# Optimization experiments

Hardware: AMD Instinct MI355X
Metric: run time of the kernel (lower is better)

Reference implementation:

```python
import jax, jax.numpy as jnp
import numpy as np

VAR = (0.1, 0.2)        # SSD encoding variances
THRESH = 0.5            # overlap_thresh
NEGPOS = 3              # neg:pos ratio


def _point_form(p):
    # (cx,cy,w,h) -> (x1,y1,x2,y2)
    return jnp.concatenate([p[:, :2] - p[:, 2:] / 2, p[:, :2] + p[:, 2:] / 2], axis=1)


def _jaccard(a, b):
    # a: [O,4], b: [P,4], corner form -> IoU [O,P]
    lt = jnp.maximum(a[:, None, :2], b[None, :, :2])
    rb = jnp.minimum(a[:, None, 2:], b[None, :, 2:])
    wh = jnp.maximum(rb - lt, 0.0)
    inter = wh[..., 0] * wh[..., 1]
    area_a = ((a[:, 2] - a[:, 0]) * (a[:, 3] - a[:, 1]))[:, None]
    area_b = ((b[:, 2] - b[:, 0]) * (b[:, 3] - b[:, 1]))[None, :]
    return inter / (area_a + area_b - inter)


def _encode(matched, priors):
    # matched: [P,4] corner form, priors: [P,4] center form
    g_cxcy = ((matched[:, :2] + matched[:, 2:]) / 2 - priors[:, :2]) / (VAR[0] * priors[:, 2:])
    g_wh = jnp.log((matched[:, 2:] - matched[:, :2]) / priors[:, 2:]) / VAR[1]
    return jnp.concatenate([g_cxcy, g_wh], axis=1)


def _match(truths, labels, priors):
    # truths: [O,4], labels: [O], priors: [P,4] -> loc_t [P,4], conf_t [P], obj_t [P]
    O = truths.shape[0]
    over = _jaccard(truths, _point_form(priors))          # [O,P]
    best_prior_idx = jnp.argmax(over, axis=1)             # [O] best prior per truth
    best_truth_overlap = over.max(axis=0)                 # [P]
    best_truth_idx = jnp.argmax(over, axis=0)             # [P]
    best_truth_overlap = best_truth_overlap.at[best_prior_idx].set(2.0)
    best_truth_idx = best_truth_idx.at[best_prior_idx].set(jnp.arange(O))
    matched = truths[best_truth_idx]                      # [P,4]
    conf = labels[best_truth_idx].astype(jnp.int32) + 1   # background = 0
    conf = jnp.where(best_truth_overlap < THRESH, 0, conf)
    return _encode(matched, priors), conf, conf > 0


def _ce(logits, tgt):
    # per-element cross entropy, logits [...,C], tgt [...] int
    return jax.nn.logsumexp(logits, axis=-1) - jnp.take_along_axis(logits, tgt[..., None], axis=-1)[..., 0]


def _mine_neg(loss, pos, P):
    # hard negative mining via double argsort (rank of each elem in descending loss order)
    loss = jnp.where(pos, 0.0, loss)
    loss_idx = jnp.argsort(-loss, axis=1)
    idx_rank = jnp.argsort(loss_idx, axis=1)
    num_neg = jnp.minimum(NEGPOS * pos.sum(axis=1, keepdims=True), P - 1)
    return idx_rank < num_neg


def setup_inputs() -> dict:
    key = jax.random.key(0)
    ks = jax.random.split(key, 8)
    B, P, C, O = 64, 16320, 81, 50
    loc_data = jax.random.normal(ks[0], (B, P, 4), jnp.float32)
    conf_data = jax.random.normal(ks[1], (B, P, C), jnp.float32)
    obj_data = jax.random.normal(ks[2], (B, P, 2), jnp.float32)
    # priors: center form, positive w/h
    cxcy = jax.random.uniform(ks[3], (P, 2), minval=0.05, maxval=0.95)
    wh = jax.random.uniform(ks[4], (P, 2), minval=0.02, maxval=0.3)
    priors = jnp.concatenate([cxcy, wh], axis=1).astype(jnp.float32)
    # targets: valid corner-form boxes + float label in last column
    tc = jax.random.uniform(ks[5], (B, O, 2), minval=0.1, maxval=0.9)
    twh = jax.random.uniform(ks[6], (B, O, 2), minval=0.05, maxval=0.3)
    boxes = jnp.concatenate([jnp.clip(tc - twh / 2, 0.0, 1.0), jnp.clip(tc + twh / 2, 0.0, 1.0)], axis=-1)
    labels = jax.random.randint(ks[7], (B, O), 0, C).astype(jnp.float32)
    targets = jnp.concatenate([boxes, labels[..., None]], axis=-1).astype(jnp.float32)
    return {"loc_data": loc_data, "conf_data": conf_data, "obj_data": obj_data,
            "priors": priors, "targets": targets}


def reference(loc_data, conf_data, obj_data, priors, targets):
    B, P, C = conf_data.shape
    loc_t, conf_t, pos = jax.vmap(lambda t: _match(t[:, :4], t[:, 4], priors))(targets)
    loc_t = jax.lax.stop_gradient(loc_t)  # torch builds targets detached

    # localization: smooth L1 over positives, sum reduction
    d = loc_data - loc_t
    sl1 = jnp.where(jnp.abs(d) < 1.0, 0.5 * d * d, jnp.abs(d) - 0.5)
    loss_l = jnp.sum(sl1 * pos[..., None].astype(sl1.dtype))

    # combined (C+1)-way logit: col0 = obj_bg + log(sum(exp(conf))), cols 1..C = obj_fg + conf
    lse_conf = jax.nn.logsumexp(conf_data, axis=-1)                        # [B,P]
    logit = jnp.concatenate([(obj_data[..., 0] + lse_conf)[..., None],
                             obj_data[..., 1:2] + conf_data], axis=-1)     # [B,P,C+1]

    ce_c = _ce(logit, conf_t)                       # [B,P]
    neg_c = _mine_neg(ce_c, pos, P)
    loss_c = jnp.sum(jnp.where(pos | neg_c, ce_c, 0.0))

    ce_o = _ce(obj_data, pos.astype(jnp.int32))     # [B,P]
    neg_o = _mine_neg(ce_o, pos, P)
    loss_obj = jnp.sum(jnp.where(pos | neg_o, ce_o, 0.0))

    N = pos.sum().astype(jnp.float32)
    return loss_l / N, loss_c / N, loss_obj / N
```

## Files before the change

kernel.cpp:

```cpp
#include <hip/hip_runtime.h>
#include <cstdint>
#include <cstddef>

#define THRESH   0.5f
#define NEGPOS   3
#define VAR0     0.1f
#define VAR1     0.2f
#define MAXO     64
#define NPRI     8
#define A1_T     256
#define MINE_T   1024
#define MINE_W   (MINE_T / 64)
#define HCOPIES  8

__global__ __launch_bounds__(A1_T)
void match_kernel(const float* __restrict__ priors,
                  const float* __restrict__ targets,
                  unsigned char* __restrict__ code,
                  unsigned long long* __restrict__ g_bp,
                  int B, int P, int O, int chunks) {
    __shared__ float tx1[MAXO], ty1[MAXO], tx2[MAXO], ty2[MAXO], tarea[MAXO];
    const int b   = blockIdx.x / chunks;
    const int ch  = blockIdx.x % chunks;
    const int tid = threadIdx.x;

    if (tid < O) {
        const float* tr = targets + (size_t)(b * O + tid) * 5;
        float x1 = tr[0], y1 = tr[1], x2 = tr[2], y2 = tr[3];
        tx1[tid] = x1; ty1[tid] = y1; tx2[tid] = x2; ty2[tid] = y2;
        tarea[tid] = (x2 - x1) * (y2 - y1);
    }
    __syncthreads();

    float px1[NPRI], py1[NPRI], px2[NPRI], py2[NPRI], pa[NPRI], pov[NPRI];
    int   pidx[NPRI];
    const int p0 = ch * (A1_T * NPRI) + tid;
#pragma unroll
    for (int i = 0; i < NPRI; ++i) {
        int p = p0 + i * A1_T;
        pov[i] = -1.0f; pidx[i] = 0;
        px1[i] = 0.f; py1[i] = 0.f; px2[i] = 0.f; py2[i] = 0.f; pa[i] = 1.0f;
        if (p < P) {
            float4 pr = *(const float4*)(priors + (size_t)p * 4);
            px1[i] = pr.x - pr.z * 0.5f; py1[i] = pr.y - pr.w * 0.5f;
            px2[i] = pr.x + pr.z * 0.5f; py2[i] = pr.y + pr.w * 0.5f;
            pa[i]  = pr.z * pr.w;
        }
    }

    const int lane = tid & 63;
    for (int o = 0; o < O; ++o) {
        float ax1 = tx1[o], ay1 = ty1[o], ax2 = tx2[o], ay2 = ty2[o], aa = tarea[o];
        float bo = -1.0f; unsigned bp = 0u;
#pragma unroll
        for (int i = 0; i < NPRI; ++i) {
            float lx = fmaxf(ax1, px1[i]), ly = fmaxf(ay1, py1[i]);
            float rx = fminf(ax2, px2[i]), ry = fminf(ay2, py2[i]);
            float w = fmaxf(rx - lx, 0.0f), h = fmaxf(ry - ly, 0.0f);
            float inter = w * h;
            float iou = __fdividef(inter, aa + pa[i] - inter);
            if (iou > pov[i]) { pov[i] = iou; pidx[i] = o; }
            if (iou > bo)     { bo = iou; bp = (unsigned)(p0 + i * A1_T); }
        }
        unsigned long long key =
            ((unsigned long long)__float_as_uint(bo) << 32) |
            (unsigned long long)(0xFFFFFFFFu - bp);
#pragma unroll
        for (int d = 1; d < 64; d <<= 1) {
            unsigned long long other = __shfl_xor(key, d, 64);
            if (other > key) key = other;
        }
        if (lane == 0)
            atomicMax(&g_bp[(size_t)b * O + o], key);
    }

#pragma unroll
    for (int i = 0; i < NPRI; ++i) {
        int p = p0 + i * A1_T;
        if (p < P)
            code[(size_t)b * P + p] =
                (pov[i] >= THRESH) ? (unsigned char)(pidx[i] + 1) : (unsigned char)0;
    }
}

__global__ void force_kernel(const unsigned long long* __restrict__ g_bp,
                             unsigned char* __restrict__ code,
                             int B, int P, int O) {
    int b = blockIdx.x * blockDim.x + threadIdx.x;
    if (b >= B) return;
    for (int o = 0; o < O; ++o) {
        unsigned long long key = g_bp[(size_t)b * O + o];
        unsigned p = 0xFFFFFFFFu - (unsigned)(key & 0xFFFFFFFFull);
        code[(size_t)b * P + p] = (unsigned char)(o + 1);
    }
}

__global__ __launch_bounds__(256)
void ce_pos_kernel(const float* __restrict__ loc, const float* __restrict__ conf,
                   const float* __restrict__ obj, const float* __restrict__ priors,
                   const float* __restrict__ targets,
                   const unsigned char* __restrict__ code,
                   float* __restrict__ mce, float* __restrict__ rowacc,
                   int B, int P, int C, int O) {
    const int b = blockIdx.y;
    const int p = blockIdx.x * 256 + threadIdx.x;
    const int tid = threadIdx.x, wv = tid >> 6, lane = tid & 63;

    bool pos = false;
    unsigned cc = 0;
    const unsigned t = (unsigned)(b * P + p);
    float obx = 0.f, oby = 0.f, lse2 = 0.f;
    if (p < P) {
        cc = code[t];
        float2 ob = *(const float2*)(obj + (size_t)t * 2);
        obx = ob.x; oby = ob.y;
        float m = fmaxf(obx, oby);
        lse2 = m + __logf(__expf(obx - m) + __expf(oby - m));
        if (cc == 0) {
            mce[t] = lse2 - obx;
        } else {
            mce[t] = 0.0f;
            pos = true;
        }
    }

    const unsigned long long msk = __ballot(pos);
    float myS = 0.f;
    unsigned long long rem = msk;
    while (rem) {
        const int src = __ffsll(rem) - 1;
        rem &= rem - 1;
        const unsigned t_s = (unsigned)__shfl((int)t, src, 64);
        const float* cr = conf + (size_t)t_s * C;
        float s = 0.f;
        for (int j = lane; j < C; j += 64) s += __expf(cr[j]);
#pragma unroll
        for (int d = 1; d < 64; d <<= 1) s += __shfl_xor(s, d, 64);
        if (lane == src) myS = s;
    }

    float sl = 0.f, cec = 0.f, ceo = 0.f;
    if (pos) {
        const float* cr = conf + (size_t)t * C;
        const float* tr = targets + (size_t)((unsigned)(b * O) + cc - 1u) * 5;
        float4 pr = *(const float4*)(priors + (size_t)p * 4);
        float4 ld = *(const float4*)(loc + (size_t)t * 4);
        float mx1 = tr[0], my1 = tr[1], mx2 = tr[2], my2 = tr[3];
        int   lbl = (int)tr[4];

        float lsec = __logf(myS);
        cec = lsec + lse2 - oby - cr[lbl];
        ceo = lse2 - oby;

        float gx  = ((mx1 + mx2) * 0.5f - pr.x) / (VAR0 * pr.z);
        float gy  = ((my1 + my2) * 0.5f - pr.y) / (VAR0 * pr.w);
        float gw2 = __logf((mx2 - mx1) / pr.z) / VAR1;
        float gh  = __logf((my2 - my1) / pr.w) / VAR1;
        float d0 = ld.x - gx,  a0 = fabsf(d0); sl += (a0 < 1.f) ? 0.5f * d0 * d0 : a0 - 0.5f;
        float d1 = ld.y - gy,  a1 = fabsf(d1); sl += (a1 < 1.f) ? 0.5f * d1 * d1 : a1 - 0.5f;
        float d2 = ld.z - gw2, a2 = fabsf(d2); sl += (a2 < 1.f) ? 0.5f * d2 * d2 : a2 - 0.5f;
        float d3 = ld.w - gh,  a3 = fabsf(d3); sl += (a3 < 1.f) ? 0.5f * d3 * d3 : a3 - 0.5f;
    }

    float cntp = (float)__popcll(msk);
    __shared__ float red[4][4];
#pragma unroll
    for (int d = 32; d > 0; d >>= 1) {
        sl  += __shfl_down(sl,  d, 64);
        cec += __shfl_down(cec, d, 64);
        ceo += __shfl_down(ceo, d, 64);
    }
    if (lane == 0) {
        red[wv][0] = cntp; red[wv][1] = sl; red[wv][2] = cec; red[wv][3] = ceo;
    }
    __syncthreads();
    if (tid < 4) {
        float v = red[0][tid] + red[1][tid] + red[2][tid] + red[3][tid];
        if (v != 0.0f)
            atomicAdd(rowacc + (size_t)b * 16 + tid, v);
    }
}

__global__ __launch_bounds__(MINE_T)
void mine_kernel(const float* __restrict__ mce, const float* __restrict__ rowacc,
                 float* __restrict__ g_neg, int P) {
    const int b = blockIdx.x;
    const float* row = mce + (size_t)b * P;
    int npos = (int)rowacc[(size_t)b * 16];
    int k = NEGPOS * npos;
    if (k > P - 1) k = P - 1;
    if (k <= 0) return;

    __shared__ unsigned hist[HCOPIES][257];
    __shared__ unsigned s_prefix;
    __shared__ int      s_rem;
    __shared__ float    s_ws[MINE_W];
    __shared__ int      s_wc[MINE_W];

    const int tid  = threadIdx.x;
    const int wv   = tid >> 6;
    const int hc   = wv & (HCOPIES - 1);
    const int lane = tid & 63;

    unsigned prefix = 0u;
    int rem = k;
    for (int shift = 24; shift >= 0; shift -= 8) {
        for (int i = tid; i < HCOPIES * 257; i += MINE_T) (&hist[0][0])[i] = 0u;
        __syncthreads();
        unsigned himask = (shift == 24) ? 0u : (0xFFFFFFFFu << (shift + 8));
        for (int i = tid; i < P; i += MINE_T) {
            unsigned bits = __float_as_uint(row[i]);
            if ((bits & himask) == prefix)
                atomicAdd(&hist[hc][(bits >> shift) & 0xFFu], 1u);
        }
        __syncthreads();
        if (tid == 0) {
            int cum = 0; unsigned bin = 0;
            for (int bb = 255; bb >= 0; --bb) {
                int cnt = 0;
#pragma unroll
                for (int h = 0; h < HCOPIES; ++h) cnt += (int)hist[h][bb];
                if (cum + cnt >= rem) { bin = (unsigned)bb; rem -= cum; break; }
                cum += cnt;
            }
            s_prefix = prefix | (bin << shift);
            s_rem = rem;
        }
        __syncthreads();
        prefix = s_prefix;
        rem    = s_rem;
    }

    float vk = __uint_as_float(prefix);
    float s = 0.f; int cnt = 0;
    for (int i = tid; i < P; i += MINE_T) {
        float v = row[i];
        if (__float_as_uint(v) > prefix) { s += v; ++cnt; }
    }
#pragma unroll
    for (int d = 32; d > 0; d >>= 1) {
        s   += __shfl_down(s, d, 64);
        cnt += __shfl_down(cnt, d, 64);
    }
    if (lane == 0) { s_ws[wv] = s; s_wc[wv] = cnt; }
    __syncthreads();
    if (tid == 0) {
        float st = 0.f; int ct = 0;
        for (int w = 0; w < MINE_W; ++w) { st += s_ws[w]; ct += s_wc[w]; }
        atomicAdd(g_neg, st + (float)(k - ct) * vk);
    }
}

__global__ void finish_kernel(const float* __restrict__ rowacc,
                              const float* __restrict__ g_neg,
                              float* __restrict__ out, int B) {
    const int lane = threadIdx.x;
    float npos = 0.f, sl = 0.f, cec = 0.f, ceo = 0.f;
    for (int b = lane; b < B; b += 64) {
        float4 v = *(const float4*)(rowacc + (size_t)b * 16);
        npos += v.x; sl += v.y; cec += v.z; ceo += v.w;
    }
#pragma unroll
    for (int d = 32; d > 0; d >>= 1) {
        npos += __shfl_down(npos, d, 64);
        sl   += __shfl_down(sl,   d, 64);
        cec  += __shfl_down(cec,  d, 64);
        ceo  += __shfl_down(ceo,  d, 64);
    }
    if (lane == 0) {
        float neg = *g_neg;
        out[0] = sl / npos;
        out[1] = (cec + neg) / npos;
        out[2] = (ceo + neg) / npos;
    }
}

extern "C" void kernel_launch(void* const* d_in, const int* in_sizes, int n_in,
                              void* d_out, int out_size, void* d_ws, size_t ws_size,
                              hipStream_t stream) {
    const float* loc     = (const float*)d_in[0];
    const float* conf    = (const float*)d_in[1];
    const float* obj     = (const float*)d_in[2];
    const float* priors  = (const float*)d_in[3];
    const float* targets = (const float*)d_in[4];

    const int P = in_sizes[3] / 4;
    const int B = in_sizes[0] / (4 * P);
    const int C = in_sizes[1] / (B * P);
    const int O = in_sizes[4] / (5 * B);

    char* ws = (char*)d_ws;
    size_t off = 0;
    float* g_neg = (float*)(ws + off);             off += 64;
    float* rowacc = (float*)(ws + off);            off += (size_t)B * 16 * sizeof(float);
    unsigned long long* g_bp = (unsigned long long*)(ws + off);
    off += (size_t)B * O * sizeof(unsigned long long);
    const size_t zero_bytes = off;
    off = (off + 127) & ~(size_t)127;
    unsigned char* code = (unsigned char*)(ws + off); off += (size_t)B * P;
    off = (off + 127) & ~(size_t)127;
    float* mce = (float*)(ws + off);               off += (size_t)B * P * sizeof(float);

    hipMemsetAsync(d_ws, 0, zero_bytes, stream);

    const int chunks = (P + A1_T * NPRI - 1) / (A1_T * NPRI);
    match_kernel<<<B * chunks, A1_T, 0, stream>>>(priors, targets, code, g_bp,
                                                  B, P, O, chunks);
    force_kernel<<<(B + 63) / 64, 64, 0, stream>>>(g_bp, code, B, P, O);
    dim3 ce_grid((P + 255) / 256, B);
    ce_pos_kernel<<<ce_grid, 256, 0, stream>>>(loc, conf, obj, priors, targets,
                                               code, mce, rowacc, B, P, C, O);
    mine_kernel<<<B, MINE_T, 0, stream>>>(mce, rowacc, g_neg, P);
    finish_kernel<<<1, 64, 0, stream>>>(rowacc, g_neg, (float*)d_out, B);
}
```

Measured before the change: 585.6 us.

## Fuse CE and hard-negative mining into one per-row kernel with value histogram

```diff
diff --git a/kernel.cpp b/kernel.cpp
--- a/kernel.cpp
+++ b/kernel.cpp
@@ -9,20 +9,22 @@
 #define MAXO     64
 #define NPRI     8
 #define A1_T     256
-#define MINE_T   1024
-#define MINE_W   (MINE_T / 64)
-#define HCOPIES  8
+#define ROW_T    1024
+#define NBIN     4096
+#define CAP      4096
 
 __global__ __launch_bounds__(A1_T)
 void match_kernel(const float* __restrict__ priors,
                   const float* __restrict__ targets,
                   unsigned char* __restrict__ code,
-                  unsigned long long* __restrict__ g_bp,
+                  unsigned long long* __restrict__ g_bp2,
                   int B, int P, int O, int chunks) {
     __shared__ float tx1[MAXO], ty1[MAXO], tx2[MAXO], ty2[MAXO], tarea[MAXO];
+    __shared__ unsigned long long wkeys[(A1_T / 64) * MAXO];
     const int b   = blockIdx.x / chunks;
     const int ch  = blockIdx.x % chunks;
     const int tid = threadIdx.x;
+    const int lane = tid & 63, wv = tid >> 6;
 
     if (tid < O) {
         const float* tr = targets + (size_t)(b * O + tid) * 5;
@@ -48,7 +50,6 @@
         }
     }
 
-    const int lane = tid & 63;
     for (int o = 0; o < O; ++o) {
         float ax1 = tx1[o], ay1 = ty1[o], ax2 = tx2[o], ay2 = ty2[o], aa = tarea[o];
         float bo = -1.0f; unsigned bp = 0u;
@@ -70,8 +71,17 @@
             unsigned long long other = __shfl_xor(key, d, 64);
             if (other > key) key = other;
         }
-        if (lane == 0)
-            atomicMax(&g_bp[(size_t)b * O + o], key);
+        if (lane == 0) wkeys[wv * MAXO + o] = key;
+    }
+    __syncthreads();
+    if (tid < O) {
+        unsigned long long k = wkeys[tid];
+#pragma unroll
+        for (int w = 1; w < A1_T / 64; ++w) {
+            unsigned long long o2 = wkeys[w * MAXO + tid];
+            if (o2 > k) k = o2;
+        }
+        g_bp2[(size_t)(b * chunks + ch) * MAXO + tid] = k;
     }
 
 #pragma unroll
@@ -83,182 +93,211 @@
     }
 }
 
-__global__ void force_kernel(const unsigned long long* __restrict__ g_bp,
-                             unsigned char* __restrict__ code,
-                             int B, int P, int O) {
-    int b = blockIdx.x * blockDim.x + threadIdx.x;
-    if (b >= B) return;
-    for (int o = 0; o < O; ++o) {
-        unsigned long long key = g_bp[(size_t)b * O + o];
-        unsigned p = 0xFFFFFFFFu - (unsigned)(key & 0xFFFFFFFFull);
-        code[(size_t)b * P + p] = (unsigned char)(o + 1);
-    }
-}
-
-__global__ __launch_bounds__(256)
-void ce_pos_kernel(const float* __restrict__ loc, const float* __restrict__ conf,
-                   const float* __restrict__ obj, const float* __restrict__ priors,
-                   const float* __restrict__ targets,
-                   const unsigned char* __restrict__ code,
-                   float* __restrict__ mce, float* __restrict__ rowacc,
-                   int B, int P, int C, int O) {
-    const int b = blockIdx.y;
-    const int p = blockIdx.x * 256 + threadIdx.x;
-    const int tid = threadIdx.x, wv = tid >> 6, lane = tid & 63;
-
-    bool pos = false;
-    unsigned cc = 0;
-    const unsigned t = (unsigned)(b * P + p);
-    float obx = 0.f, oby = 0.f, lse2 = 0.f;
-    if (p < P) {
-        cc = code[t];
-        float2 ob = *(const float2*)(obj + (size_t)t * 2);
-        obx = ob.x; oby = ob.y;
-        float m = fmaxf(obx, oby);
-        lse2 = m + __logf(__expf(obx - m) + __expf(oby - m));
+__global__ __launch_bounds__(64)
+void force_kernel(const unsigned long long* __restrict__ g_bp2,
+                  unsigned char* __restrict__ code,
+                  int P, int O, int chunks) {
+    const int b = blockIdx.x, o = threadIdx.x;
+    __shared__ unsigned s_p[MAXO];
+    unsigned p = 0xFFFFFFFFu;
+    if (o < O) {
+        unsigned long long k = 0ull;
+        for (int ch = 0; ch < chunks; ++ch) {
+            unsigned long long v = g_bp2[(size_t)(b * chunks + ch) * MAXO + o];
+            if (v > k) k = v;
+        }
+        p = 0xFFFFFFFFu - (unsigned)(k & 0xFFFFFFFFull);
+        s_p[o] = p;
+    }
+    __syncthreads();
+    if (o < O) {
+        bool last = true;
+        for (int o2 = o + 1; o2 < O; ++o2)
+            if (s_p[o2] == p) { last = false; break; }
+        if (last) code[(size_t)b * P + p] = (unsigned char)(o + 1);
+    }
+}
+
+__global__ __launch_bounds__(ROW_T)
+void row_kernel(const float* __restrict__ loc, const float* __restrict__ conf,
+                const float* __restrict__ obj, const float* __restrict__ priors,
+                const float* __restrict__ targets,
+                const unsigned char* __restrict__ code,
+                float* __restrict__ rowout, int P, int C, int O) {
+    const int b = blockIdx.x;
+    const int tid = threadIdx.x;
+    const int lane = tid & 63, wv = tid >> 6;
+
+    __shared__ unsigned hist[NBIN];
+    __shared__ int s_idx[CAP];
+    __shared__ int s_np, s_nc, s_bound, s_rem;
+    __shared__ int wavetot[ROW_T / 64], wexc[ROW_T / 64];
+    __shared__ float red[ROW_T / 64][4];
+
+    for (int i = tid; i < NBIN; i += ROW_T) hist[i] = 0u;
+    if (tid == 0) { s_np = 0; s_nc = 0; s_bound = NBIN; s_rem = 0; }
+    __syncthreads();
+
+    const size_t rowbase = (size_t)b * P;
+
+    for (int i = tid; i < P; i += ROW_T) {
+        unsigned cc = code[rowbase + i];
+        float2 ob = *(const float2*)(obj + (rowbase + i) * 2);
+        float m = fmaxf(ob.x, ob.y);
+        float lse2 = m + __logf(__expf(ob.x - m) + __expf(ob.y - m));
+        float v = 0.0f;
         if (cc == 0) {
-            mce[t] = lse2 - obx;
+            v = lse2 - ob.x;
         } else {
-            mce[t] = 0.0f;
-            pos = true;
-        }
-    }
-
-    const unsigned long long msk = __ballot(pos);
-    float myS = 0.f;
-    unsigned long long rem = msk;
-    while (rem) {
-        const int src = __ffsll(rem) - 1;
-        rem &= rem - 1;
-        const unsigned t_s = (unsigned)__shfl((int)t, src, 64);
-        const float* cr = conf + (size_t)t_s * C;
-        float s = 0.f;
-        for (int j = lane; j < C; j += 64) s += __expf(cr[j]);
-#pragma unroll
-        for (int d = 1; d < 64; d <<= 1) s += __shfl_xor(s, d, 64);
-        if (lane == src) myS = s;
-    }
-
-    float sl = 0.f, cec = 0.f, ceo = 0.f;
-    if (pos) {
-        const float* cr = conf + (size_t)t * C;
-        const float* tr = targets + (size_t)((unsigned)(b * O) + cc - 1u) * 5;
-        float4 pr = *(const float4*)(priors + (size_t)p * 4);
-        float4 ld = *(const float4*)(loc + (size_t)t * 4);
-        float mx1 = tr[0], my1 = tr[1], mx2 = tr[2], my2 = tr[3];
-        int   lbl = (int)tr[4];
-
-        float lsec = __logf(myS);
-        cec = lsec + lse2 - oby - cr[lbl];
-        ceo = lse2 - oby;
-
-        float gx  = ((mx1 + mx2) * 0.5f - pr.x) / (VAR0 * pr.z);
-        float gy  = ((my1 + my2) * 0.5f - pr.y) / (VAR0 * pr.w);
-        float gw2 = __logf((mx2 - mx1) / pr.z) / VAR1;
-        float gh  = __logf((my2 - my1) / pr.w) / VAR1;
-        float d0 = ld.x - gx,  a0 = fabsf(d0); sl += (a0 < 1.f) ? 0.5f * d0 * d0 : a0 - 0.5f;
-        float d1 = ld.y - gy,  a1 = fabsf(d1); sl += (a1 < 1.f) ? 0.5f * d1 * d1 : a1 - 0.5f;
-        float d2 = ld.z - gw2, a2 = fabsf(d2); sl += (a2 < 1.f) ? 0.5f * d2 * d2 : a2 - 0.5f;
-        float d3 = ld.w - gh,  a3 = fabsf(d3); sl += (a3 < 1.f) ? 0.5f * d3 * d3 : a3 - 0.5f;
-    }
-
-    float cntp = (float)__popcll(msk);
-    __shared__ float red[4][4];
+            int s = atomicAdd(&s_np, 1);
+            if (s < CAP) s_idx[s] = (i << 8) | (int)cc;
+        }
+        int bin = (int)(v * 512.0f);
+        bin = min(bin, NBIN - 1);
+        atomicAdd(&hist[bin], 1u);
+    }
+    __syncthreads();
+    const int np = s_np;
+
+    float sl = 0.f, cec = 0.f, ceo = 0.f, neg = 0.f;
+
+    {
+        const int unit = tid >> 4, lq = tid & 15;
+        for (int j = unit; j < np; j += ROW_T / 16) {
+            int pk = s_idx[j];
+            int p  = pk >> 8, cc = pk & 0xFF;
+            size_t t = rowbase + (size_t)p;
+            const float* cr = conf + t * C;
+            float s = 0.f;
+            for (int c = lq; c < C; c += 16) s += __expf(cr[c]);
+#pragma unroll
+            for (int d = 1; d < 16; d <<= 1) s += __shfl_xor(s, d, 16);
+            if (lq == 0) {
+                const float* tr = targets + (size_t)(b * O + cc - 1) * 5;
+                float2 ob = *(const float2*)(obj + t * 2);
+                float m = fmaxf(ob.x, ob.y);
+                float lse2 = m + __logf(__expf(ob.x - m) + __expf(ob.y - m));
+                int lbl = (int)tr[4];
+                cec += __logf(s) + lse2 - ob.y - cr[lbl];
+                ceo += lse2 - ob.y;
+                float4 pr = *(const float4*)(priors + (size_t)p * 4);
+                float4 ld = *(const float4*)(loc + t * 4);
+                float mx1 = tr[0], my1 = tr[1], mx2 = tr[2], my2 = tr[3];
+                float gx  = ((mx1 + mx2) * 0.5f - pr.x) / (VAR0 * pr.z);
+                float gy  = ((my1 + my2) * 0.5f - pr.y) / (VAR0 * pr.w);
+                float gw2 = __logf((mx2 - mx1) / pr.z) / VAR1;
+                float gh  = __logf((my2 - my1) / pr.w) / VAR1;
+                float d0 = ld.x - gx,  a0 = fabsf(d0); sl += (a0 < 1.f) ? 0.5f*d0*d0 : a0 - 0.5f;
+                float d1 = ld.y - gy,  a1 = fabsf(d1); sl += (a1 < 1.f) ? 0.5f*d1*d1 : a1 - 0.5f;
+                float d2 = ld.z - gw2, a2 = fabsf(d2); sl += (a2 < 1.f) ? 0.5f*d2*d2 : a2 - 0.5f;
+                float d3 = ld.w - gh,  a3 = fabsf(d3); sl += (a3 < 1.f) ? 0.5f*d3*d3 : a3 - 0.5f;
+            }
+        }
+    }
+    __syncthreads();
+
+    int k = NEGPOS * np;
+    if (k > P - 1) k = P - 1;
+    if (k > 0) {
+        const int base = NBIN - 1 - 4 * tid;
+        const int c0 = (int)hist[base],     c1 = (int)hist[base - 1];
+        const int c2 = (int)hist[base - 2], c3 = (int)hist[base - 3];
+        const int T = c0 + c1 + c2 + c3;
+        int incl = T;
+#pragma unroll
+        for (int d = 1; d < 64; d <<= 1) {
+            int vv = __shfl_up(incl, d, 64);
+            if (lane >= d) incl += vv;
+        }
+        if (lane == 63) wavetot[wv] = incl;
+        __syncthreads();
+        if (wv == 0 && lane < ROW_T / 64) {
+            int t2 = wavetot[lane], inc2 = t2;
+#pragma unroll
+            for (int d = 1; d < 16; d <<= 1) {
+                int vv = __shfl_up(inc2, d, 16);
+                if ((lane & 15) >= d) inc2 += vv;
+            }
+            wexc[lane] = inc2 - t2;
+        }
+        __syncthreads();
+        const int E = wexc[wv] + incl - T;
+        if (E < k && E + T >= k) {
+            int bound, rem;
+            if      (E + c0 >= k)           { bound = base;     rem = k - E; }
+            else if (E + c0 + c1 >= k)      { bound = base - 1; rem = k - E - c0; }
+            else if (E + c0 + c1 + c2 >= k) { bound = base - 2; rem = k - E - c0 - c1; }
+            else                            { bound = base - 3; rem = k - E - c0 - c1 - c2; }
+            s_bound = bound; s_rem = rem;
+        }
+    }
+    __syncthreads();
+    const int bound = s_bound, rem = s_rem;
+
+    if (k > 0) {
+        for (int i = tid; i < P; i += ROW_T) {
+            unsigned cc = code[rowbase + i];
+            if (cc) continue;
+            float2 ob = *(const float2*)(obj + (rowbase + i) * 2);
+            float m = fmaxf(ob.x, ob.y);
+            float v = m + __logf(__expf(ob.x - m) + __expf(ob.y - m)) - ob.x;
+            int bin = (int)(v * 512.0f);
+            bin = min(bin, NBIN - 1);
+            if (bin > bound) {
+                neg += v;
+            } else if (bin == bound) {
+                int c = atomicAdd(&s_nc, 1);
+                if (c < CAP) s_idx[c] = __float_as_int(v);
+            }
+        }
+    }
+    __syncthreads();
+
+    if (k > 0) {
+        int n = s_nc; if (n > CAP) n = CAP;
+        if (n <= rem) {
+            for (int i = tid; i < n; i += ROW_T) neg += __int_as_float(s_idx[i]);
+        } else {
+            for (int i = tid; i < n; i += ROW_T) {
+                unsigned bi = (unsigned)s_idx[i];
+                int g = 0, e = 0;
+                for (int j = 0; j < n; ++j) {
+                    unsigned bj = (unsigned)s_idx[j];
+                    g += (bj > bi);
+                    e += (j < i && bj == bi);
+                }
+                if (g + e < rem) neg += __int_as_float((int)bi);
+            }
+        }
+    }
+
 #pragma unroll
     for (int d = 32; d > 0; d >>= 1) {
         sl  += __shfl_down(sl,  d, 64);
         cec += __shfl_down(cec, d, 64);
         ceo += __shfl_down(ceo, d, 64);
-    }
-    if (lane == 0) {
-        red[wv][0] = cntp; red[wv][1] = sl; red[wv][2] = cec; red[wv][3] = ceo;
-    }
-    __syncthreads();
-    if (tid < 4) {
-        float v = red[0][tid] + red[1][tid] + red[2][tid] + red[3][tid];
-        if (v != 0.0f)
-            atomicAdd(rowacc + (size_t)b * 16 + tid, v);
-    }
-}
-
-__global__ __launch_bounds__(MINE_T)
-void mine_kernel(const float* __restrict__ mce, const float* __restrict__ rowacc,
-                 float* __restrict__ g_neg, int P) {
-    const int b = blockIdx.x;
-    const float* row = mce + (size_t)b * P;
-    int npos = (int)rowacc[(size_t)b * 16];
-    int k = NEGPOS * npos;
-    if (k > P - 1) k = P - 1;
-    if (k <= 0) return;
-
-    __shared__ unsigned hist[HCOPIES][257];
-    __shared__ unsigned s_prefix;
-    __shared__ int      s_rem;
-    __shared__ float    s_ws[MINE_W];
-    __shared__ int      s_wc[MINE_W];
-
-    const int tid  = threadIdx.x;
-    const int wv   = tid >> 6;
-    const int hc   = wv & (HCOPIES - 1);
-    const int lane = tid & 63;
-
-    unsigned prefix = 0u;
-    int rem = k;
-    for (int shift = 24; shift >= 0; shift -= 8) {
-        for (int i = tid; i < HCOPIES * 257; i += MINE_T) (&hist[0][0])[i] = 0u;
-        __syncthreads();
-        unsigned himask = (shift == 24) ? 0u : (0xFFFFFFFFu << (shift + 8));
-        for (int i = tid; i < P; i += MINE_T) {
-            unsigned bits = __float_as_uint(row[i]);
-            if ((bits & himask) == prefix)
-                atomicAdd(&hist[hc][(bits >> shift) & 0xFFu], 1u);
-        }
-        __syncthreads();
-        if (tid == 0) {
-            int cum = 0; unsigned bin = 0;
-            for (int bb = 255; bb >= 0; --bb) {
-                int cnt = 0;
-#pragma unroll
-                for (int h = 0; h < HCOPIES; ++h) cnt += (int)hist[h][bb];
-                if (cum + cnt >= rem) { bin = (unsigned)bb; rem -= cum; break; }
-                cum += cnt;
-            }
-            s_prefix = prefix | (bin << shift);
-            s_rem = rem;
-        }
-        __syncthreads();
-        prefix = s_prefix;
-        rem    = s_rem;
-    }
-
-    float vk = __uint_as_float(prefix);
-    float s = 0.f; int cnt = 0;
-    for (int i = tid; i < P; i += MINE_T) {
-        float v = row[i];
-        if (__float_as_uint(v) > prefix) { s += v; ++cnt; }
-    }
-#pragma unroll
-    for (int d = 32; d > 0; d >>= 1) {
-        s   += __shfl_down(s, d, 64);
-        cnt += __shfl_down(cnt, d, 64);
-    }
-    if (lane == 0) { s_ws[wv] = s; s_wc[wv] = cnt; }
+        neg += __shfl_down(neg, d, 64);
+    }
+    if (lane == 0) { red[wv][0] = sl; red[wv][1] = cec; red[wv][2] = ceo; red[wv][3] = neg; }
     __syncthreads();
     if (tid == 0) {
-        float st = 0.f; int ct = 0;
-        for (int w = 0; w < MINE_W; ++w) { st += s_ws[w]; ct += s_wc[w]; }
-        atomicAdd(g_neg, st + (float)(k - ct) * vk);
-    }
-}
-
-__global__ void finish_kernel(const float* __restrict__ rowacc,
-                              const float* __restrict__ g_neg,
-                              float* __restrict__ out, int B) {
+        float a0 = 0.f, a1 = 0.f, a2 = 0.f, a3 = 0.f;
+        for (int w = 0; w < ROW_T / 64; ++w) {
+            a0 += red[w][0]; a1 += red[w][1]; a2 += red[w][2]; a3 += red[w][3];
+        }
+        float* ro = rowout + (size_t)b * 8;
+        ro[0] = (float)np; ro[1] = a0; ro[2] = a1; ro[3] = a2; ro[4] = a3;
+    }
+}
+
+__global__ __launch_bounds__(64)
+void finish_kernel(const float* __restrict__ rowout,
+                   float* __restrict__ out, int B) {
     const int lane = threadIdx.x;
-    float npos = 0.f, sl = 0.f, cec = 0.f, ceo = 0.f;
+    float npos = 0.f, sl = 0.f, cec = 0.f, ceo = 0.f, neg = 0.f;
     for (int b = lane; b < B; b += 64) {
-        float4 v = *(const float4*)(rowacc + (size_t)b * 16);
-        npos += v.x; sl += v.y; cec += v.z; ceo += v.w;
+        const float* ro = rowout + (size_t)b * 8;
+        npos += ro[0]; sl += ro[1]; cec += ro[2]; ceo += ro[3]; neg += ro[4];
     }
 #pragma unroll
     for (int d = 32; d > 0; d >>= 1) {
@@ -266,9 +305,9 @@
         sl   += __shfl_down(sl,   d, 64);
         cec  += __shfl_down(cec,  d, 64);
         ceo  += __shfl_down(ceo,  d, 64);
+        neg  += __shfl_down(neg,  d, 64);
     }
     if (lane == 0) {
-        float neg = *g_neg;
         out[0] = sl / npos;
         out[1] = (cec + neg) / npos;
         out[2] = (ceo + neg) / npos;
@@ -289,27 +328,20 @@
     const int C = in_sizes[1] / (B * P);
     const int O = in_sizes[4] / (5 * B);
 
+    const int chunks = (P + A1_T * NPRI - 1) / (A1_T * NPRI);
+
     char* ws = (char*)d_ws;
     size_t off = 0;
-    float* g_neg = (float*)(ws + off);             off += 64;
-    float* rowacc = (float*)(ws + off);            off += (size_t)B * 16 * sizeof(float);
-    unsigned long long* g_bp = (unsigned long long*)(ws + off);
-    off += (size_t)B * O * sizeof(unsigned long long);
-    const size_t zero_bytes = off;
-    off = (off + 127) & ~(size_t)127;
+    unsigned long long* g_bp2 = (unsigned long long*)(ws + off);
+    off += (size_t)B * chunks * MAXO * sizeof(unsigned long long);
+    float* rowout = (float*)(ws + off);            off += (size_t)B * 8 * sizeof(float);
     unsigned char* code = (unsigned char*)(ws + off); off += (size_t)B * P;
-    off = (off + 127) & ~(size_t)127;
-    float* mce = (float*)(ws + off);               off += (size_t)B * P * sizeof(float);
-
-    hipMemsetAsync(d_ws, 0, zero_bytes, stream);
-
-    const int chunks = (P + A1_T * NPRI - 1) / (A1_T * NPRI);
-    match_kernel<<<B * chunks, A1_T, 0, stream>>>(priors, targets, code, g_bp,
+
+
+    match_kernel<<<B * chunks, A1_T, 0, stream>>>(priors, targets, code, g_bp2,
                                                   B, P, O, chunks);
-    force_kernel<<<(B + 63) / 64, 64, 0, stream>>>(g_bp, code, B, P, O);
-    dim3 ce_grid((P + 255) / 256, B);
-    ce_pos_kernel<<<ce_grid, 256, 0, stream>>>(loc, conf, obj, priors, targets,
-                                               code, mce, rowacc, B, P, C, O);
-    mine_kernel<<<B, MINE_T, 0, stream>>>(mce, rowacc, g_neg, P);
-    finish_kernel<<<1, 64, 0, stream>>>(rowacc, g_neg, (float*)d_out, B);
-}
+    force_kernel<<<B, 64, 0, stream>>>(g_bp2, code, P, O, chunks);
+    row_kernel<<<B, ROW_T, 0, stream>>>(loc, conf, obj, priors, targets,
+                                        code, rowout, P, C, O);
+    finish_kernel<<<1, 64, 0, stream>>>(rowout, (float*)d_out, B);
+}
```

Result: slower. 604.5 us (+3.2%).
